# Kernel tuning notes

Measured on AMD Instinct MI355X. Metric: run time of the kernel, lower is better.

Reference implementation:

```python
import jax, jax.numpy as jnp
import numpy as np

B, T, IN, CELL, OUT = 512, 32, 512, 128, 128


def setup_inputs() -> dict:
    key = jax.random.key(0)
    ks = jax.random.split(key, 6)
    d = IN + CELL
    w = lambda k, shape, fan: jax.random.normal(k, shape, jnp.float32) / np.sqrt(fan).astype(np.float32)
    return {
        "x": jax.random.normal(ks[0], (B, T, IN), jnp.float32),
        "Wf": w(ks[1], (d, CELL), d), "bf": jnp.zeros((CELL,), jnp.float32),
        "Wi1": w(ks[2], (d, CELL), d), "bi1": jnp.zeros((CELL,), jnp.float32),
        "Wi2": w(ks[3], (d, CELL), d), "bi2": jnp.zeros((CELL,), jnp.float32),
        "Wo": w(ks[4], (d, CELL), d), "bo": jnp.zeros((CELL,), jnp.float32),
        "Wc": w(ks[5], (CELL, OUT), CELL), "bc": jnp.zeros((OUT,), jnp.float32),
    }


def reference(x, Wf, bf, Wi1, bi1, Wi2, bi2, Wo, bo, Wc, bc):
    # Faithful to MyLSTM.forward: loop runs x.shape[1] times; each iteration
    # concatenates the FULL [B,T,CELL] cell_state with the FULL [B,T,IN] x
    # (x is never sliced per step). Only the last iteration's output matters,
    # but we carry it through the scan to match the loop structure exactly.
    Tn = x.shape[1]
    c0 = jnp.zeros(x.shape[:2] + (Wf.shape[1],), x.dtype)
    out0 = jnp.zeros(x.shape[:2] + (Wc.shape[1],), x.dtype)

    def step(carry, _):
        c, _prev_out = carry
        inp = jnp.concatenate([c, x], axis=-1)  # [B,T,CELL+IN]
        f = jax.nn.sigmoid(inp @ Wf + bf)
        c = c * f + jax.nn.sigmoid(inp @ Wi1 + bi1) * jnp.tanh(inp @ Wi2 + bi2)
        o = jax.nn.sigmoid(inp @ Wo + bo) * jnp.tanh(c)
        out = jax.nn.softmax(o @ Wc + bc, axis=2)  # out_features != 1 branch
        return (c, out), None

    (c, out), _ = jax.lax.scan(step, (c0, out0), None, length=Tn)
    return out, c
```

## Files before the change

### kernel.cpp

```cpp
#include <hip/hip_runtime.h>
#include <stdint.h>

#define ROWS  16384
#define CELL  128
#define INF   512
#define RPB   16
#define NSTEP 32

typedef _Float16 f16x8 __attribute__((ext_vector_type(8)));
typedef _Float16 f16x4 __attribute__((ext_vector_type(4)));
typedef float    f32x4 __attribute__((ext_vector_type(4)));

#define MFMA16(a, b, c) __builtin_amdgcn_mfma_f32_16x16x32_f16((a), (b), (c), 0, 0, 0)

#define AOFF  0
#define XOFF  65536
#define WCOFF 327680
#define WSTOT 344064

#define LOG2E  1.44269504f
#define LOG2E2 2.88539008f

__device__ __forceinline__ unsigned short f2h_bits(float f) {
  _Float16 h = (_Float16)f;
  return *(unsigned short*)&h;
}
__device__ __forceinline__ float sig2(float z) {
  return __builtin_amdgcn_rcpf(1.f + __builtin_amdgcn_exp2f(-z));
}
__device__ __forceinline__ float tanh2(float z) {
  return 1.f - 2.f * __builtin_amdgcn_rcpf(__builtin_amdgcn_exp2f(z) + 1.f);
}

__global__ __launch_bounds__(256) void prep_kernel(
    const float* __restrict__ Wf, const float* __restrict__ Wi1,
    const float* __restrict__ Wi2, const float* __restrict__ Wo,
    const float* __restrict__ Wc, unsigned short* __restrict__ ws) {
  int id = blockIdx.x * blockDim.x + threadIdx.x;
  if (id >= WSTOT) return;
  const float* Wg[4] = {Wf, Wi1, Wi2, Wo};
  const float scl[4] = {LOG2E, LOG2E, LOG2E2, LOG2E};
  float v;
  int k, n, base;
  if (id < XOFF) {
    int g = id >> 14, r = id & 16383;
    k = r >> 7; n = r & 127;
    v = Wg[g][k * CELL + n] * scl[g];
    base = g * 16384;
  } else if (id < WCOFF) {
    int t = id - XOFF;
    int g = t >> 16, r = t & 65535;
    k = r >> 7; n = r & 127;
    v = Wg[g][(CELL + k) * CELL + n] * scl[g];
    base = XOFF + g * 65536;
  } else {
    int r = id - WCOFF;
    k = r >> 7; n = r & 127;
    v = Wc[k * CELL + n] * LOG2E;
    base = WCOFF;
  }
  int ks = k >> 5, kk = k & 31;
  int lane = ((kk >> 3) << 4) | (n & 15);
  int j = kk & 7, nb = n >> 4;
  ws[base + ((ks * 8 + nb) * 64 + lane) * 8 + j] = f2h_bits(v);
}

__global__ __launch_bounds__(512, 4) void lstm_kernel(
    const float* __restrict__ x,
    const float* __restrict__ bf_, const float* __restrict__ bi1,
    const float* __restrict__ bi2, const float* __restrict__ bo,
    const float* __restrict__ bc,
    const unsigned short* __restrict__ ws, float* __restrict__ out) {

  __shared__ _Float16 cF[2][16 * 128];
  __shared__ union {
    _Float16 xs[16 * 512];
    struct {
      float    e[16][132];
      _Float16 o[16 * 128];
    } ep;
  } uS;

  const int tid  = threadIdx.x;
  const int lane = tid & 63;
  const int w    = tid >> 6;
  const int n16  = lane & 15;
  const int g4   = lane >> 4;
  const int sxor = n16 & 7;
  const int col0 = w * 16 + g4 * 4;
  const int r0   = blockIdx.x * RPB;

  const _Float16* Aw  = (const _Float16*)ws + AOFF;
  const _Float16* Xw  = (const _Float16*)ws + XOFF;
  const _Float16* Wcw = (const _Float16*)ws + WCOFF;

  int aoff[4];
#pragma unroll
  for (int ks = 0; ks < 4; ++ks)
    aoff[ks] = n16 * 128 + (((4 * ks + g4) ^ sxor) << 3);
  const int woff = n16 * 128 + (((2 * w + (g4 >> 1)) ^ sxor) << 3) + (g4 & 1) * 4;

  {
    const float* xb = x + (size_t)r0 * INF;
#pragma unroll
    for (int i = 0; i < 4; ++i) {
      int flat = tid + i * 512;
      int row = flat >> 7, c4 = flat & 127;
      const float4 v = ((const float4*)(xb + (size_t)row * INF))[c4];
      f16x4 h = {(_Float16)v.x, (_Float16)v.y, (_Float16)v.z, (_Float16)v.w};
      int idx = row * 512 + (((c4 >> 1) ^ (row & 7)) << 3) + (c4 & 1) * 4;
      *(f16x4*)&uS.xs[idx] = h;
    }
  }
  __syncthreads();

  f32x4 u[4];
#pragma unroll
  for (int g = 0; g < 4; ++g)
#pragma unroll
    for (int i = 0; i < 4; ++i) u[g][i] = 0.f;

#pragma unroll 4
  for (int ks = 0; ks < 16; ++ks) {
    f16x8 a = *(const f16x8*)&uS.xs[n16 * 512 + (((4 * ks + g4) ^ sxor) << 3)];
#pragma unroll
    for (int g = 0; g < 4; ++g) {
      f16x8 b = *(const f16x8*)(Xw + g * 65536 + ((ks * 8 + w) * 64 + lane) * 8);
      u[g] = MFMA16(b, a, u[g]);
    }
  }
  {
    f32x4 b0 = *(const f32x4*)&bf_[col0];
    f32x4 b1 = *(const f32x4*)&bi1[col0];
    f32x4 b2 = *(const f32x4*)&bi2[col0];
    f32x4 b3 = *(const f32x4*)&bo[col0];
#pragma unroll
    for (int i = 0; i < 4; ++i) {
      u[0][i] = fmaf(b0[i], LOG2E,  u[0][i]);
      u[1][i] = fmaf(b1[i], LOG2E,  u[1][i]);
      u[2][i] = fmaf(b2[i], LOG2E2, u[2][i]);
      u[3][i] = fmaf(b3[i], LOG2E,  u[3][i]);
    }
  }

  f16x8 wr[3][4];
#pragma unroll
  for (int g = 0; g < 3; ++g)
#pragma unroll
    for (int ks = 0; ks < 4; ++ks)
      wr[g][ks] = *(const f16x8*)(Aw + g * 16384 + ((ks * 8 + w) * 64 + lane) * 8);

  f32x4 cr;
  {
    f16x4 hv;
#pragma unroll
    for (int i = 0; i < 4; ++i) {
      float c0 = sig2(u[1][i]) * tanh2(u[2][i]);
      cr[i] = c0;
      hv[i] = (_Float16)c0;
    }
    *(f16x4*)&cF[0][woff] = hv;
  }
  __syncthreads();

#pragma unroll 1
  for (int t = 1; t < NSTEP - 1; ++t) {
    const _Float16* rd = cF[(t + 1) & 1];
    f16x8 a0 = *(const f16x8*)(rd + aoff[0]);
    f16x8 a1 = *(const f16x8*)(rd + aoff[1]);
    f16x8 a2 = *(const f16x8*)(rd + aoff[2]);
    f16x8 a3 = *(const f16x8*)(rd + aoff[3]);
    f32x4 zf  = MFMA16(wr[0][0], a0, u[0]);
    f32x4 zi1 = MFMA16(wr[1][0], a0, u[1]);
    f32x4 zi2 = MFMA16(wr[2][0], a0, u[2]);
    zf  = MFMA16(wr[0][1], a1, zf);
    zi1 = MFMA16(wr[1][1], a1, zi1);
    zi2 = MFMA16(wr[2][1], a1, zi2);
    zf  = MFMA16(wr[0][2], a2, zf);
    zi1 = MFMA16(wr[1][2], a2, zi1);
    zi2 = MFMA16(wr[2][2], a2, zi2);
    zf  = MFMA16(wr[0][3], a3, zf);
    zi1 = MFMA16(wr[1][3], a3, zi1);
    zi2 = MFMA16(wr[2][3], a3, zi2);
    f16x4 hv;
#pragma unroll
    for (int i = 0; i < 4; ++i) {
      float fg = sig2(zf[i]);
      float ig = sig2(zi1[i]);
      float gg = tanh2(zi2[i]);
      float cn = fmaf(cr[i], fg, ig * gg);
      cr[i] = cn;
      hv[i] = (_Float16)cn;
    }
    *(f16x4*)&cF[t & 1][woff] = hv;
    __syncthreads();
  }

  {
    const _Float16* rd = cF[0];
    f16x8 a0 = *(const f16x8*)(rd + aoff[0]);
    f16x8 a1 = *(const f16x8*)(rd + aoff[1]);
    f16x8 a2 = *(const f16x8*)(rd + aoff[2]);
    f16x8 a3 = *(const f16x8*)(rd + aoff[3]);
    f16x8 bo0 = *(const f16x8*)(Aw + 3 * 16384 + ((0 * 8 + w) * 64 + lane) * 8);
    f16x8 bo1 = *(const f16x8*)(Aw + 3 * 16384 + ((1 * 8 + w) * 64 + lane) * 8);
    f16x8 bo2 = *(const f16x8*)(Aw + 3 * 16384 + ((2 * 8 + w) * 64 + lane) * 8);
    f16x8 bo3 = *(const f16x8*)(Aw + 3 * 16384 + ((3 * 8 + w) * 64 + lane) * 8);
    f32x4 zf  = MFMA16(wr[0][0], a0, u[0]);
    f32x4 zi1 = MFMA16(wr[1][0], a0, u[1]);
    f32x4 zi2 = MFMA16(wr[2][0], a0, u[2]);
    f32x4 zo  = MFMA16(bo0,      a0, u[3]);
    zf  = MFMA16(wr[0][1], a1, zf);
    zi1 = MFMA16(wr[1][1], a1, zi1);
    zi2 = MFMA16(wr[2][1], a1, zi2);
    zo  = MFMA16(bo1,      a1, zo);
    zf  = MFMA16(wr[0][2], a2, zf);
    zi1 = MFMA16(wr[1][2], a2, zi1);
    zi2 = MFMA16(wr[2][2], a2, zi2);
    zo  = MFMA16(bo2,      a2, zo);
    zf  = MFMA16(wr[0][3], a3, zf);
    zi1 = MFMA16(wr[1][3], a3, zi1);
    zi2 = MFMA16(wr[2][3], a3, zi2);
    zo  = MFMA16(bo3,      a3, zo);
    f16x4 hv;
#pragma unroll
    for (int i = 0; i < 4; ++i) {
      float fg = sig2(zf[i]);
      float ig = sig2(zi1[i]);
      float gg = tanh2(zi2[i]);
      float cn = fmaf(cr[i], fg, ig * gg);
      cr[i] = cn;
      float ov = sig2(zo[i]) * tanh2(cn * LOG2E2);
      hv[i] = (_Float16)ov;
    }
    *(f16x4*)&uS.ep.o[woff] = hv;
    __syncthreads();
  }

  {
    f32x4 sacc;
#pragma unroll
    for (int i = 0; i < 4; ++i) sacc[i] = 0.f;
#pragma unroll
    for (int ks = 0; ks < 4; ++ks) {
      f16x8 a = *(const f16x8*)&uS.ep.o[aoff[ks]];
      f16x8 b = *(const f16x8*)(Wcw + ((ks * 8 + w) * 64 + lane) * 8);
      sacc = MFMA16(b, a, sacc);
    }
    f32x4 bcv = *(const f32x4*)&bc[col0];
    f32x4 ev;
#pragma unroll
    for (int i = 0; i < 4; ++i)
      ev[i] = __builtin_amdgcn_exp2f(fmaf(bcv[i], LOG2E, sacc[i]));
    *(f32x4*)&uS.ep.e[n16][col0] = ev;
    __syncthreads();

#pragma unroll
    for (int rr = 0; rr < 2; ++rr) {
      int r = w * 2 + rr;
      float e0 = uS.ep.e[r][lane];
      float e1 = uS.ep.e[r][lane + 64];
      float sm = e0 + e1;
#pragma unroll
      for (int off = 32; off; off >>= 1) sm += __shfl_xor(sm, off, 64);
      float inv = __builtin_amdgcn_rcpf(sm);
      size_t base = (size_t)(r0 + r) * 128;
      out[base + lane]      = e0 * inv;
      out[base + lane + 64] = e1 * inv;
    }

    *(f32x4*)&out[(size_t)ROWS * 128 + (size_t)(r0 + n16) * 128 + col0] = cr;
  }
}

extern "C" void kernel_launch(void* const* d_in, const int* in_sizes, int n_in,
                              void* d_out, int out_size, void* d_ws, size_t ws_size,
                              hipStream_t stream) {
  const float* x   = (const float*)d_in[0];
  const float* Wf  = (const float*)d_in[1];
  const float* bf_ = (const float*)d_in[2];
  const float* Wi1 = (const float*)d_in[3];
  const float* bi1 = (const float*)d_in[4];
  const float* Wi2 = (const float*)d_in[5];
  const float* bi2 = (const float*)d_in[6];
  const float* Wo  = (const float*)d_in[7];
  const float* bo  = (const float*)d_in[8];
  const float* Wc  = (const float*)d_in[9];
  const float* bc  = (const float*)d_in[10];
  unsigned short* ws = (unsigned short*)d_ws;
  float* out = (float*)d_out;

  hipLaunchKernelGGL(prep_kernel, dim3((WSTOT + 255) / 256), dim3(256), 0, stream,
                     Wf, Wi1, Wi2, Wo, Wc, ws);
  hipLaunchKernelGGL(lstm_kernel, dim3(ROWS / RPB), dim3(512), 0, stream,
                     x, bf_, bi1, bi2, bo, bc, ws, out);
}
```

Measured before the change: 167.8 us.

## Process two 16-row tiles per block to reuse recurrent weights and interleave MFMA chains

Each block now handles 32 rows instead of 16, computing two independent 16-row recurrences that share the same register-resident recurrent weights and input-projection weight loads. The two tiles' MFMA chains and gate math are interleaved within each time step, so one tile's activations can overlap with the other's matrix work, and the per-step barrier is paid once for twice the rows. The output-gate projection is parked in shared memory to limit register pressure. In exchange, register and LDS use per block rise, which may lower occupancy, and the grid is halved.

```diff
diff --git a/kernel.cpp b/kernel.cpp
--- a/kernel.cpp
+++ b/kernel.cpp
@@ -4,7 +4,7 @@
 #define ROWS  16384
 #define CELL  128
 #define INF   512
-#define RPB   16
+#define RPB   32
 #define NSTEP 32
 
 typedef _Float16 f16x8 __attribute__((ext_vector_type(8)));
@@ -72,12 +72,12 @@
     const float* __restrict__ bc,
     const unsigned short* __restrict__ ws, float* __restrict__ out) {
 
-  __shared__ _Float16 cF[2][16 * 128];
+  __shared__ _Float16 cF[2][32 * 128];
   __shared__ union {
-    _Float16 xs[16 * 512];
+    _Float16 xs[32 * 512];
     struct {
-      float    e[16][132];
-      _Float16 o[16 * 128];
+      float    ue[32][132];
+      _Float16 o[32 * 128];
     } ep;
   } uS;
 
@@ -103,7 +103,7 @@
   {
     const float* xb = x + (size_t)r0 * INF;
 #pragma unroll
-    for (int i = 0; i < 4; ++i) {
+    for (int i = 0; i < 8; ++i) {
       int flat = tid + i * 512;
       int row = flat >> 7, c4 = flat & 127;
       const float4 v = ((const float4*)(xb + (size_t)row * INF))[c4];
@@ -114,19 +114,28 @@
   }
   __syncthreads();
 
-  f32x4 u[4];
-#pragma unroll
-  for (int g = 0; g < 4; ++g)
-#pragma unroll
-    for (int i = 0; i < 4; ++i) u[g][i] = 0.f;
-
-#pragma unroll 4
+  f32x4 u[2][4];
+#pragma unroll
+  for (int h = 0; h < 2; ++h)
+#pragma unroll
+    for (int g = 0; g < 4; ++g)
+#pragma unroll
+      for (int i = 0; i < 4; ++i) u[h][g][i] = 0.f;
+
+#pragma unroll 2
   for (int ks = 0; ks < 16; ++ks) {
-    f16x8 a = *(const f16x8*)&uS.xs[n16 * 512 + (((4 * ks + g4) ^ sxor) << 3)];
-#pragma unroll
-    for (int g = 0; g < 4; ++g) {
-      f16x8 b = *(const f16x8*)(Xw + g * 65536 + ((ks * 8 + w) * 64 + lane) * 8);
-      u[g] = MFMA16(b, a, u[g]);
+    f16x8 b0 = *(const f16x8*)(Xw + 0 * 65536 + ((ks * 8 + w) * 64 + lane) * 8);
+    f16x8 b1 = *(const f16x8*)(Xw + 1 * 65536 + ((ks * 8 + w) * 64 + lane) * 8);
+    f16x8 b2 = *(const f16x8*)(Xw + 2 * 65536 + ((ks * 8 + w) * 64 + lane) * 8);
+    f16x8 b3 = *(const f16x8*)(Xw + 3 * 65536 + ((ks * 8 + w) * 64 + lane) * 8);
+#pragma unroll
+    for (int h = 0; h < 2; ++h) {
+      f16x8 a = *(const f16x8*)&uS.xs[(h * 16 + n16) * 512 +
+                                      (((4 * ks + g4) ^ sxor) << 3)];
+      u[h][0] = MFMA16(b0, a, u[h][0]);
+      u[h][1] = MFMA16(b1, a, u[h][1]);
+      u[h][2] = MFMA16(b2, a, u[h][2]);
+      u[h][3] = MFMA16(b3, a, u[h][3]);
     }
   }
   {
@@ -135,13 +144,19 @@
     f32x4 b2 = *(const f32x4*)&bi2[col0];
     f32x4 b3 = *(const f32x4*)&bo[col0];
 #pragma unroll
-    for (int i = 0; i < 4; ++i) {
-      u[0][i] = fmaf(b0[i], LOG2E,  u[0][i]);
-      u[1][i] = fmaf(b1[i], LOG2E,  u[1][i]);
-      u[2][i] = fmaf(b2[i], LOG2E2, u[2][i]);
-      u[3][i] = fmaf(b3[i], LOG2E,  u[3][i]);
-    }
-  }
+    for (int h = 0; h < 2; ++h)
+#pragma unroll
+      for (int i = 0; i < 4; ++i) {
+        u[h][0][i] = fmaf(b0[i], LOG2E,  u[h][0][i]);
+        u[h][1][i] = fmaf(b1[i], LOG2E,  u[h][1][i]);
+        u[h][2][i] = fmaf(b2[i], LOG2E2, u[h][2][i]);
+        u[h][3][i] = fmaf(b3[i], LOG2E,  u[h][3][i]);
+      }
+  }
+  __syncthreads();
+
+  *(f32x4*)&uS.ep.ue[n16][col0]      = u[0][3];
+  *(f32x4*)&uS.ep.ue[16 + n16][col0] = u[1][3];
 
   f16x8 wr[3][4];
 #pragma unroll
@@ -150,29 +165,37 @@
     for (int ks = 0; ks < 4; ++ks)
       wr[g][ks] = *(const f16x8*)(Aw + g * 16384 + ((ks * 8 + w) * 64 + lane) * 8);
 
-  f32x4 cr;
+  f32x4 cr0, cr1;
   {
     f16x4 hv;
 #pragma unroll
     for (int i = 0; i < 4; ++i) {
-      float c0 = sig2(u[1][i]) * tanh2(u[2][i]);
-      cr[i] = c0;
+      float c0 = sig2(u[0][1][i]) * tanh2(u[0][2][i]);
+      cr0[i] = c0;
       hv[i] = (_Float16)c0;
     }
     *(f16x4*)&cF[0][woff] = hv;
+#pragma unroll
+    for (int i = 0; i < 4; ++i) {
+      float c0 = sig2(u[1][1][i]) * tanh2(u[1][2][i]);
+      cr1[i] = c0;
+      hv[i] = (_Float16)c0;
+    }
+    *(f16x4*)&cF[0][2048 + woff] = hv;
   }
   __syncthreads();
 
 #pragma unroll 1
   for (int t = 1; t < NSTEP - 1; ++t) {
     const _Float16* rd = cF[(t + 1) & 1];
+    _Float16*       wp = cF[t & 1];
     f16x8 a0 = *(const f16x8*)(rd + aoff[0]);
     f16x8 a1 = *(const f16x8*)(rd + aoff[1]);
     f16x8 a2 = *(const f16x8*)(rd + aoff[2]);
     f16x8 a3 = *(const f16x8*)(rd + aoff[3]);
-    f32x4 zf  = MFMA16(wr[0][0], a0, u[0]);
-    f32x4 zi1 = MFMA16(wr[1][0], a0, u[1]);
-    f32x4 zi2 = MFMA16(wr[2][0], a0, u[2]);
+    f32x4 zf  = MFMA16(wr[0][0], a0, u[0][0]);
+    f32x4 zi1 = MFMA16(wr[1][0], a0, u[0][1]);
+    f32x4 zi2 = MFMA16(wr[2][0], a0, u[0][2]);
     zf  = MFMA16(wr[0][1], a1, zf);
     zi1 = MFMA16(wr[1][1], a1, zi1);
     zi2 = MFMA16(wr[2][1], a1, zi2);
@@ -182,84 +205,126 @@
     zf  = MFMA16(wr[0][3], a3, zf);
     zi1 = MFMA16(wr[1][3], a3, zi1);
     zi2 = MFMA16(wr[2][3], a3, zi2);
-    f16x4 hv;
-#pragma unroll
-    for (int i = 0; i < 4; ++i) {
-      float fg = sig2(zf[i]);
-      float ig = sig2(zi1[i]);
-      float gg = tanh2(zi2[i]);
-      float cn = fmaf(cr[i], fg, ig * gg);
-      cr[i] = cn;
-      hv[i] = (_Float16)cn;
-    }
-    *(f16x4*)&cF[t & 1][woff] = hv;
+    f16x8 e0 = *(const f16x8*)(rd + 2048 + aoff[0]);
+    f16x8 e1 = *(const f16x8*)(rd + 2048 + aoff[1]);
+    f16x8 e2 = *(const f16x8*)(rd + 2048 + aoff[2]);
+    f16x8 e3 = *(const f16x8*)(rd + 2048 + aoff[3]);
+    {
+      f16x4 hv;
+#pragma unroll
+      for (int i = 0; i < 4; ++i) {
+        float fg = sig2(zf[i]);
+        float ig = sig2(zi1[i]);
+        float gg = tanh2(zi2[i]);
+        float cn = fmaf(cr0[i], fg, ig * gg);
+        cr0[i] = cn;
+        hv[i] = (_Float16)cn;
+      }
+      *(f16x4*)&wp[woff] = hv;
+    }
+    zf  = MFMA16(wr[0][0], e0, u[1][0]);
+    zi1 = MFMA16(wr[1][0], e0, u[1][1]);
+    zi2 = MFMA16(wr[2][0], e0, u[1][2]);
+    zf  = MFMA16(wr[0][1], e1, zf);
+    zi1 = MFMA16(wr[1][1], e1, zi1);
+    zi2 = MFMA16(wr[2][1], e1, zi2);
+    zf  = MFMA16(wr[0][2], e2, zf);
+    zi1 = MFMA16(wr[1][2], e2, zi1);
+    zi2 = MFMA16(wr[2][2], e2, zi2);
+    zf  = MFMA16(wr[0][3], e3, zf);
+    zi1 = MFMA16(wr[1][3], e3, zi1);
+    zi2 = MFMA16(wr[2][3], e3, zi2);
+    {
+      f16x4 hv;
+#pragma unroll
+      for (int i = 0; i < 4; ++i) {
+        float fg = sig2(zf[i]);
+        float ig = sig2(zi1[i]);
+        float gg = tanh2(zi2[i]);
+        float cn = fmaf(cr1[i], fg, ig * gg);
+        cr1[i] = cn;
+        hv[i] = (_Float16)cn;
+      }
+      *(f16x4*)&wp[2048 + woff] = hv;
+    }
     __syncthreads();
   }
 
   {
     const _Float16* rd = cF[0];
-    f16x8 a0 = *(const f16x8*)(rd + aoff[0]);
-    f16x8 a1 = *(const f16x8*)(rd + aoff[1]);
-    f16x8 a2 = *(const f16x8*)(rd + aoff[2]);
-    f16x8 a3 = *(const f16x8*)(rd + aoff[3]);
     f16x8 bo0 = *(const f16x8*)(Aw + 3 * 16384 + ((0 * 8 + w) * 64 + lane) * 8);
     f16x8 bo1 = *(const f16x8*)(Aw + 3 * 16384 + ((1 * 8 + w) * 64 + lane) * 8);
     f16x8 bo2 = *(const f16x8*)(Aw + 3 * 16384 + ((2 * 8 + w) * 64 + lane) * 8);
     f16x8 bo3 = *(const f16x8*)(Aw + 3 * 16384 + ((3 * 8 + w) * 64 + lane) * 8);
-    f32x4 zf  = MFMA16(wr[0][0], a0, u[0]);
-    f32x4 zi1 = MFMA16(wr[1][0], a0, u[1]);
-    f32x4 zi2 = MFMA16(wr[2][0], a0, u[2]);
-    f32x4 zo  = MFMA16(bo0,      a0, u[3]);
-    zf  = MFMA16(wr[0][1], a1, zf);
-    zi1 = MFMA16(wr[1][1], a1, zi1);
-    zi2 = MFMA16(wr[2][1], a1, zi2);
-    zo  = MFMA16(bo1,      a1, zo);
-    zf  = MFMA16(wr[0][2], a2, zf);
-    zi1 = MFMA16(wr[1][2], a2, zi1);
-    zi2 = MFMA16(wr[2][2], a2, zi2);
-    zo  = MFMA16(bo2,      a2, zo);
-    zf  = MFMA16(wr[0][3], a3, zf);
-    zi1 = MFMA16(wr[1][3], a3, zi1);
-    zi2 = MFMA16(wr[2][3], a3, zi2);
-    zo  = MFMA16(bo3,      a3, zo);
-    f16x4 hv;
+#pragma unroll
+    for (int h = 0; h < 2; ++h) {
+      const int hoff = h * 2048;
+      f16x8 a0 = *(const f16x8*)(rd + hoff + aoff[0]);
+      f16x8 a1 = *(const f16x8*)(rd + hoff + aoff[1]);
+      f16x8 a2 = *(const f16x8*)(rd + hoff + aoff[2]);
+      f16x8 a3 = *(const f16x8*)(rd + hoff + aoff[3]);
+      f32x4 zos = *(const f32x4*)&uS.ep.ue[h * 16 + n16][col0];
+      f32x4 zf  = MFMA16(wr[0][0], a0, u[h][0]);
+      f32x4 zi1 = MFMA16(wr[1][0], a0, u[h][1]);
+      f32x4 zi2 = MFMA16(wr[2][0], a0, u[h][2]);
+      f32x4 zo  = MFMA16(bo0,      a0, zos);
+      zf  = MFMA16(wr[0][1], a1, zf);
+      zi1 = MFMA16(wr[1][1], a1, zi1);
+      zi2 = MFMA16(wr[2][1], a1, zi2);
+      zo  = MFMA16(bo1,      a1, zo);
+      zf  = MFMA16(wr[0][2], a2, zf);
+      zi1 = MFMA16(wr[1][2], a2, zi1);
+      zi2 = MFMA16(wr[2][2], a2, zi2);
+      zo  = MFMA16(bo2,      a2, zo);
+      zf  = MFMA16(wr[0][3], a3, zf);
+      zi1 = MFMA16(wr[1][3], a3, zi1);
+      zi2 = MFMA16(wr[2][3], a3, zi2);
+      zo  = MFMA16(bo3,      a3, zo);
+      f16x4 hv;
+      f32x4& cr = h ? cr1 : cr0;
+#pragma unroll
+      for (int i = 0; i < 4; ++i) {
+        float fg = sig2(zf[i]);
+        float ig = sig2(zi1[i]);
+        float gg = tanh2(zi2[i]);
+        float cn = fmaf(cr[i], fg, ig * gg);
+        cr[i] = cn;
+        float ov = sig2(zo[i]) * tanh2(cn * LOG2E2);
+        hv[i] = (_Float16)ov;
+      }
+      *(f16x4*)&uS.ep.o[hoff + woff] = hv;
+    }
+  }
+  __syncthreads();
+
+  {
+    f32x4 s0, s1;
+#pragma unroll
+    for (int i = 0; i < 4; ++i) { s0[i] = 0.f; s1[i] = 0.f; }
+#pragma unroll
+    for (int ks = 0; ks < 4; ++ks) {
+      f16x8 bW = *(const f16x8*)(Wcw + ((ks * 8 + w) * 64 + lane) * 8);
+      f16x8 oa = *(const f16x8*)&uS.ep.o[aoff[ks]];
+      f16x8 ob = *(const f16x8*)&uS.ep.o[2048 + aoff[ks]];
+      s0 = MFMA16(bW, oa, s0);
+      s1 = MFMA16(bW, ob, s1);
+    }
+    f32x4 bcv = *(const f32x4*)&bc[col0];
+    f32x4 ev0, ev1;
 #pragma unroll
     for (int i = 0; i < 4; ++i) {
-      float fg = sig2(zf[i]);
-      float ig = sig2(zi1[i]);
-      float gg = tanh2(zi2[i]);
-      float cn = fmaf(cr[i], fg, ig * gg);
-      cr[i] = cn;
-      float ov = sig2(zo[i]) * tanh2(cn * LOG2E2);
-      hv[i] = (_Float16)ov;
-    }
-    *(f16x4*)&uS.ep.o[woff] = hv;
+      ev0[i] = __builtin_amdgcn_exp2f(fmaf(bcv[i], LOG2E, s0[i]));
+      ev1[i] = __builtin_amdgcn_exp2f(fmaf(bcv[i], LOG2E, s1[i]));
+    }
+    *(f32x4*)&uS.ep.ue[n16][col0]      = ev0;
+    *(f32x4*)&uS.ep.ue[16 + n16][col0] = ev1;
     __syncthreads();
-  }
-
-  {
-    f32x4 sacc;
-#pragma unroll
-    for (int i = 0; i < 4; ++i) sacc[i] = 0.f;
-#pragma unroll
-    for (int ks = 0; ks < 4; ++ks) {
-      f16x8 a = *(const f16x8*)&uS.ep.o[aoff[ks]];
-      f16x8 b = *(const f16x8*)(Wcw + ((ks * 8 + w) * 64 + lane) * 8);
-      sacc = MFMA16(b, a, sacc);
-    }
-    f32x4 bcv = *(const f32x4*)&bc[col0];
-    f32x4 ev;
-#pragma unroll
-    for (int i = 0; i < 4; ++i)
-      ev[i] = __builtin_amdgcn_exp2f(fmaf(bcv[i], LOG2E, sacc[i]));
-    *(f32x4*)&uS.ep.e[n16][col0] = ev;
-    __syncthreads();
-
-#pragma unroll
-    for (int rr = 0; rr < 2; ++rr) {
-      int r = w * 2 + rr;
-      float e0 = uS.ep.e[r][lane];
-      float e1 = uS.ep.e[r][lane + 64];
+
+#pragma unroll
+    for (int rr = 0; rr < 4; ++rr) {
+      int r = w * 4 + rr;
+      float e0 = uS.ep.ue[r][lane];
+      float e1 = uS.ep.ue[r][lane + 64];
       float sm = e0 + e1;
 #pragma unroll
       for (int off = 32; off; off >>= 1) sm += __shfl_xor(sm, off, 64);
@@ -269,7 +334,8 @@
       out[base + lane + 64] = e1 * inv;
     }
 
-    *(f32x4*)&out[(size_t)ROWS * 128 + (size_t)(r0 + n16) * 128 + col0] = cr;
+    *(f32x4*)&out[(size_t)ROWS * 128 + (size_t)(r0 + n16) * 128 + col0] = cr0;
+    *(f32x4*)&out[(size_t)ROWS * 128 + (size_t)(r0 + 16 + n16) * 128 + col0] = cr1;
   }
 }
 
```

After: 167.9 us. Within noise of the previous version (+0.1%).
